# Performance work log

Measured on AMD Instinct MI355X. Metric: run time of the kernel, lower is better.

Reference implementation:

```python
import jax, jax.numpy as jnp
import numpy as np

EPS = 1e-5

def _bn(x, g, b, m, v):
    # x: [B, C, S]; per-channel affine batchnorm in eval mode
    scale = (g * jax.lax.rsqrt(v + EPS))[None, :, None]
    return (x - m[None, :, None]) * scale + b[None, :, None]

def setup_inputs() -> dict:
    key = jax.random.key(0)
    ks = jax.random.split(key, 32)
    B, C, H, W = 8, 512, 64, 32
    IC = 64        # inter_channel = 512 // 8
    S = H * W      # in_spatial = 2048
    IS = S // 8    # inter_spatial = 256
    DS = IS // 8   # down = 32
    randn = lambda k, shp: jax.random.normal(k, shp, dtype=jnp.float32)
    rand = lambda k, shp: jax.random.uniform(k, shp, dtype=jnp.float32)
    return {
        'x': randn(ks[0], (B, C, H, W)),
        'Wt': randn(ks[1], (IC, C)) * 0.05,
        'tg': rand(ks[2], (IC,)), 'tb': randn(ks[3], (IC,)) * 0.1,
        'tm': randn(ks[4], (IC,)) * 0.1, 'tv': rand(ks[5], (IC,)),
        'Wp': randn(ks[6], (IC, C)) * 0.05,
        'pg': rand(ks[7], (IC,)), 'pb': randn(ks[8], (IC,)) * 0.1,
        'pm': randn(ks[9], (IC,)) * 0.1, 'pv': rand(ks[10], (IC,)),
        'Wgg': randn(ks[11], (IS, 2 * S)) * 0.02,
        'ggg': rand(ks[12], (IS,)), 'ggb': randn(ks[13], (IS,)) * 0.1,
        'ggm': randn(ks[14], (IS,)) * 0.1, 'ggv': rand(ks[15], (IS,)),
        'W1': randn(ks[16], (DS, IS)) * 0.05,
        'w1g': rand(ks[17], (DS,)), 'w1b': randn(ks[18], (DS,)) * 0.1,
        'w1m': randn(ks[19], (DS,)) * 0.1, 'w1v': rand(ks[20], (DS,)),
        'W2': randn(ks[21], (1, DS)) * 0.1,
        'w2g': rand(ks[22], (1,)), 'w2b': randn(ks[23], (1,)) * 0.1,
        'w2m': randn(ks[24], (1,)) * 0.1, 'w2v': rand(ks[25], (1,)),
    }

def reference(x, Wt, tg, tb, tm, tv, Wp, pg, pb, pm, pv,
              Wgg, ggg, ggb, ggm, ggv, W1, w1g, w1b, w1m, w1v,
              W2, w2g, w2b, w2m, w2v):
    B, C, H, W = x.shape
    S = H * W
    xf = x.reshape(B, C, S)
    # theta / phi: 1x1 conv + BN + ReLU -> [B, IC, S]
    theta = jax.nn.relu(_bn(jnp.einsum('oc,bcs->bos', Wt, xf), tg, tb, tm, tv))
    phi = jax.nn.relu(_bn(jnp.einsum('oc,bcs->bos', Wp, xf), pg, pb, pm, pv))
    # spatial affinity: Gs[b,s,t] = sum_c theta[b,c,s] * phi[b,c,t]
    Gs = jnp.einsum('bcs,bct->bst', theta, phi)          # [B, S, S]
    # Gs_in = Gs^T (channels=phi-spatial), Gs_out = Gs (channels=theta-spatial)
    joint = jnp.concatenate([jnp.swapaxes(Gs, 1, 2), Gs], axis=1)  # [B, 2S, S]
    g = jax.nn.relu(_bn(jnp.einsum('oc,bcs->bos', Wgg, joint), ggg, ggb, ggm, ggv))
    y = jax.nn.relu(_bn(jnp.einsum('oc,bcs->bos', W1, g), w1g, w1b, w1m, w1v))
    ys = _bn(jnp.einsum('oc,bcs->bos', W2, y), w2g, w2b, w2m, w2v)  # [B, 1, S]
    gate = jax.nn.sigmoid(ys).reshape(B, 1, H, W)
    return x * gate
```

## Files before the change

kernel.cpp:

```cpp
#include <hip/hip_runtime.h>
#include <math.h>

#define EPS 1e-5f
#define B_ 8
#define C_ 512
#define S_ 2048
#define IC_ 64
#define IS_ 256
#define DS_ 32

#define OFF_THT   1024
#define OFF_PHT   (OFF_THT + S_*C_)
#define OFF_A     (OFF_PHT + S_*C_)
#define OFF_G     (OFF_A + 2*IS_*C_)
#define OFF_AP    OFF_G

using short8 = __attribute__((ext_vector_type(8))) short;
using f32x4  = __attribute__((ext_vector_type(4))) float;

__device__ __forceinline__ short f2bf(float f) {
  union { float f; unsigned u; } v; v.f = f;
  unsigned r = v.u + 0x7fffu + ((v.u >> 16) & 1u);
  return (short)(r >> 16);
}
__device__ __forceinline__ float bf2f(short h) {
  union { unsigned u; float f; } v;
  v.u = ((unsigned)(unsigned short)h) << 16;
  return v.f;
}
__device__ __forceinline__ void split8arr(const float* f, short8& hi, short8& lo) {
#pragma unroll
  for (int e = 0; e < 8; ++e) {
    short h = f2bf(f[e]);
    hi[e] = h;
    lo[e] = f2bf(f[e] - bf2f(h));
  }
}
__device__ __forceinline__ void split44(float4 a, float4 b, short8& hi, short8& lo) {
  float f[8] = {a.x, a.y, a.z, a.w, b.x, b.y, b.z, b.w};
  split8arr(f, hi, lo);
}

__global__ __launch_bounds__(512) void k1_mfma(
    const float* __restrict__ x, const float* __restrict__ Wt,
    const float* __restrict__ Wp,
    const float* __restrict__ tg, const float* __restrict__ tb,
    const float* __restrict__ tm, const float* __restrict__ tv,
    const float* __restrict__ pg, const float* __restrict__ pb,
    const float* __restrict__ pm, const float* __restrict__ pv,
    float* __restrict__ thetaT, float* __restrict__ phiT) {
  __shared__ short xh[64 * 72], xlo[64 * 72];
  __shared__ short wh[2][64 * 72], wlo[2][64 * 72];
  __shared__ float cst_l[256];
  const int tid  = threadIdx.x;
  const int lane = tid & 63;
  const int wv   = tid >> 6;
  const int mat  = wv >> 2, sh = wv & 3;
  const int s0   = blockIdx.x * 64;
  const int b    = blockIdx.y;
  const float* xb = x + (size_t)b * C_ * S_;
  const int xs = tid & 63;
  const int xo = tid >> 6;

  if (tid < 64) {
    float a = tg[tid] * rsqrtf(tv[tid] + EPS);
    cst_l[tid] = a; cst_l[64 + tid] = tb[tid] - tm[tid] * a;
    float ap = pg[tid] * rsqrtf(pv[tid] + EPS);
    cst_l[128 + tid] = ap; cst_l[192 + tid] = pb[tid] - pm[tid] * ap;
  }

  float  xr[8];
  float4 wr[2][2];
  f32x4  acc[4];
#pragma unroll
  for (int i = 0; i < 4; ++i) acc[i] = (f32x4){0.f, 0.f, 0.f, 0.f};

#define K1_PF(KC) do {                                                        \
    _Pragma("unroll")                                                         \
    for (int e = 0; e < 8; ++e)                                               \
      xr[e] = xb[(size_t)((KC) + xo * 8 + e) * S_ + s0 + xs];                 \
    _Pragma("unroll")                                                         \
    for (int p = 0; p < 2; ++p) {                                             \
      int q = tid + p * 512;                                                  \
      int mq = q >> 9, m = (q >> 3) & 63, oct = q & 7;                        \
      const float* Wm = mq ? Wp : Wt;                                         \
      wr[p][0] = *(const float4*)&Wm[(size_t)m * C_ + (KC) + oct * 8];        \
      wr[p][1] = *(const float4*)&Wm[(size_t)m * C_ + (KC) + oct * 8 + 4];    \
    } } while (0)

  K1_PF(0);
  for (int c = 0; c < 8; ++c) {
    if (c) __syncthreads();
    {
      short8 hi, lo; split8arr(xr, hi, lo);
      *(short8*)&xh[xs * 72 + xo * 8]  = hi;
      *(short8*)&xlo[xs * 72 + xo * 8] = lo;
    }
#pragma unroll
    for (int p = 0; p < 2; ++p) {
      int q = tid + p * 512;
      int mq = q >> 9, m = (q >> 3) & 63, oct = q & 7;
      short8 hi, lo; split44(wr[p][0], wr[p][1], hi, lo);
      *(short8*)&wh[mq][m * 72 + oct * 8]  = hi;
      *(short8*)&wlo[mq][m * 72 + oct * 8] = lo;
    }
    __syncthreads();
    if (c < 7) K1_PF((c + 1) * 64);
#pragma unroll
    for (int ks = 0; ks < 2; ++ks) {
      const int ko = ks * 32 + ((lane >> 4) << 3);
      short8 bh, bl, ah[4], al[4];
      {
        int r = (sh * 16 + (lane & 15)) * 72 + ko;
        bh = *(const short8*)&xh[r];
        bl = *(const short8*)&xlo[r];
      }
#pragma unroll
      for (int mi = 0; mi < 4; ++mi) {
        int r = (mi * 16 + (lane & 15)) * 72 + ko;
        ah[mi] = *(const short8*)&wh[mat][r];
        al[mi] = *(const short8*)&wlo[mat][r];
      }
#pragma unroll
      for (int mi = 0; mi < 4; ++mi) {
        acc[mi] = __builtin_amdgcn_mfma_f32_16x16x32_bf16(ah[mi], bh, acc[mi], 0, 0, 0);
        acc[mi] = __builtin_amdgcn_mfma_f32_16x16x32_bf16(ah[mi], bl, acc[mi], 0, 0, 0);
        acc[mi] = __builtin_amdgcn_mfma_f32_16x16x32_bf16(al[mi], bh, acc[mi], 0, 0, 0);
      }
    }
  }
#undef K1_PF
  const float* ac = &cst_l[mat * 128];
  float* outT = mat ? phiT : thetaT;
  const int s = s0 + sh * 16 + (lane & 15);
#pragma unroll
  for (int mi = 0; mi < 4; ++mi) {
    const int m = mi * 16 + ((lane >> 4) << 2);
    float4 sc4 = *(const float4*)&ac[m];
    float4 bi4 = *(const float4*)&ac[64 + m];
    float4 q;
    q.x = fmaxf(sc4.x * acc[mi][0] + bi4.x, 0.f);
    q.y = fmaxf(sc4.y * acc[mi][1] + bi4.y, 0.f);
    q.z = fmaxf(sc4.z * acc[mi][2] + bi4.z, 0.f);
    q.w = fmaxf(sc4.w * acc[mi][3] + bi4.w, 0.f);
    *(float4*)&outT[(size_t)s * C_ + b * IC_ + m] = q;
  }
}

__global__ __launch_bounds__(256) void k2_mfma(
    const float* __restrict__ Wgg, const float* __restrict__ ws,
    float* __restrict__ Ap) {
  __shared__ short nh[64 * 72], nlo[64 * 72];
  __shared__ short oh[128 * 72], olo[128 * 72];
  const int tid  = threadIdx.x;
  const int lane = tid & 63;
  const int wv   = tid >> 6;
  const int n0    = blockIdx.x * 64;
  const int o_blk = blockIdx.y * 128;
  const int mat   = blockIdx.z >> 3;
  const int part  = blockIdx.z & 7;
  const int t0 = part * 256;
  const float* Bm = ws + (mat ? OFF_THT : OFF_PHT);
  const int xs = tid & 63;
  const int xo = tid >> 6;

  float  ar[16];
  float4 br[4][2];
  f32x4  acc[4][2];
#pragma unroll
  for (int i = 0; i < 4; ++i)
#pragma unroll
    for (int j = 0; j < 2; ++j) acc[i][j] = (f32x4){0.f, 0.f, 0.f, 0.f};

#define K2_PF(KC) do {                                                        \
    _Pragma("unroll")                                                         \
    for (int h = 0; h < 2; ++h) {                                             \
      int oct = xo + h * 4;                                                   \
      _Pragma("unroll")                                                       \
      for (int e = 0; e < 8; ++e)                                             \
        ar[h * 8 + e] = Bm[(size_t)(t0 + (KC) + oct * 8 + e) * C_ + n0 + xs]; \
    }                                                                         \
    _Pragma("unroll")                                                         \
    for (int p = 0; p < 4; ++p) {                                             \
      int q = tid + p * 256;                                                  \
      int o = q >> 3, oct = q & 7;                                            \
      const float* src = &Wgg[(size_t)(o_blk + o) * (2 * S_) + mat * S_ +     \
                              t0 + (KC) + oct * 8];                           \
      br[p][0] = *(const float4*)src;                                         \
      br[p][1] = *(const float4*)(src + 4);                                   \
    } } while (0)

  K2_PF(0);
  for (int c = 0; c < 4; ++c) {
    if (c) __syncthreads();
#pragma unroll
    for (int h = 0; h < 2; ++h) {
      int oct = xo + h * 4;
      short8 hi, lo; split8arr(&ar[h * 8], hi, lo);
      *(short8*)&nh[xs * 72 + oct * 8]  = hi;
      *(short8*)&nlo[xs * 72 + oct * 8] = lo;
    }
#pragma unroll
    for (int p = 0; p < 4; ++p) {
      int q = tid + p * 256;
      int o = q >> 3, oct = q & 7;
      short8 hi, lo; split44(br[p][0], br[p][1], hi, lo);
      *(short8*)&oh[o * 72 + oct * 8]  = hi;
      *(short8*)&olo[o * 72 + oct * 8] = lo;
    }
    __syncthreads();
    if (c < 3) K2_PF((c + 1) * 64);
#pragma unroll
    for (int ks = 0; ks < 2; ++ks) {
      const int ko = ks * 32 + ((lane >> 4) << 3);
      short8 ah[4], al[4], bh[2], bl[2];
#pragma unroll
      for (int ni = 0; ni < 4; ++ni) {
        int r = (ni * 16 + (lane & 15)) * 72 + ko;
        ah[ni] = *(const short8*)&nh[r];
        al[ni] = *(const short8*)&nlo[r];
      }
#pragma unroll
      for (int oj = 0; oj < 2; ++oj) {
        int r = (wv * 32 + oj * 16 + (lane & 15)) * 72 + ko;
        bh[oj] = *(const short8*)&oh[r];
        bl[oj] = *(const short8*)&olo[r];
      }
#pragma unroll
      for (int ni = 0; ni < 4; ++ni)
#pragma unroll
        for (int oj = 0; oj < 2; ++oj) {
          acc[ni][oj] = __builtin_amdgcn_mfma_f32_16x16x32_bf16(
              ah[ni], bh[oj], acc[ni][oj], 0, 0, 0);
          acc[ni][oj] = __builtin_amdgcn_mfma_f32_16x16x32_bf16(
              ah[ni], bl[oj], acc[ni][oj], 0, 0, 0);
          acc[ni][oj] = __builtin_amdgcn_mfma_f32_16x16x32_bf16(
              al[ni], bh[oj], acc[ni][oj], 0, 0, 0);
        }
    }
  }
#undef K2_PF
#pragma unroll
  for (int ni = 0; ni < 4; ++ni) {
    const int nq = n0 + ni * 16 + ((lane >> 4) << 2);
#pragma unroll
    for (int oj = 0; oj < 2; ++oj) {
      int o = o_blk + wv * 32 + oj * 16 + (lane & 15);
      float4 q;
      q.x = acc[ni][oj][0]; q.y = acc[ni][oj][1];
      q.z = acc[ni][oj][2]; q.w = acc[ni][oj][3];
      *(float4*)&Ap[((size_t)(part * 2 + mat) * IS_ + o) * C_ + nq] = q;
    }
  }
}

__global__ __launch_bounds__(256) void k2b_reduce(float* __restrict__ ws) {
  int f = blockIdx.x * 256 + threadIdx.x;
  const float4* ap = (const float4*)(ws + OFF_AP);
  float4* a = (float4*)(ws + OFF_A);
  float4 s = ap[f];
#pragma unroll
  for (int p = 1; p < 8; ++p) {
    float4 t = ap[f + p * 65536];
    s.x += t.x; s.y += t.y; s.z += t.z; s.w += t.w;
  }
  a[f] = s;
}

__global__ __launch_bounds__(256) void k3_mfma(
    float* __restrict__ ws,
    const float* __restrict__ gg, const float* __restrict__ gb,
    const float* __restrict__ gm, const float* __restrict__ gv) {
  __shared__ short th[64 * 72], tlo[64 * 72];
  __shared__ short ohh[128 * 72], olo[128 * 72];
  __shared__ float cstg[512];
  const int tid  = threadIdx.x;
  const int lane = tid & 63;
  const int wv   = tid >> 6;
  const int s0    = blockIdx.x * 64;
  const int o_blk = blockIdx.y * 128;
  const int b     = blockIdx.z;
  const float* A = ws + OFF_A;

  {
    float a = gg[tid] * rsqrtf(gv[tid] + EPS);
    cstg[tid] = a; cstg[256 + tid] = gb[tid] - gm[tid] * a;
  }

  float4 ar[2][2];
  float4 br[4][2];
  f32x4  acc[4][2];
#pragma unroll
  for (int i = 0; i < 4; ++i)
#pragma unroll
    for (int j = 0; j < 2; ++j) acc[i][j] = (f32x4){0.f, 0.f, 0.f, 0.f};

#define K3_PF(MAT) do {                                                       \
    const float* Tsrc = ws + ((MAT) ? OFF_PHT : OFF_THT);                     \
    _Pragma("unroll")                                                         \
    for (int p = 0; p < 2; ++p) {                                             \
      int q = tid + p * 256;                                                  \
      int sl = q >> 3, oct = q & 7;                                           \
      const float* src = &Tsrc[(size_t)(s0 + sl) * C_ + b * IC_ + oct * 8];   \
      ar[p][0] = *(const float4*)src;                                         \
      ar[p][1] = *(const float4*)(src + 4);                                   \
    }                                                                         \
    _Pragma("unroll")                                                         \
    for (int p = 0; p < 4; ++p) {                                             \
      int q = tid + p * 256;                                                  \
      int o = q >> 3, oct = q & 7;                                            \
      const float* src = &A[((size_t)(MAT) * IS_ + o_blk + o) * C_ +          \
                            b * IC_ + oct * 8];                               \
      br[p][0] = *(const float4*)src;                                         \
      br[p][1] = *(const float4*)(src + 4);                                   \
    } } while (0)

  K3_PF(0);
  for (int c = 0; c < 2; ++c) {
    if (c) __syncthreads();
#pragma unroll
    for (int p = 0; p < 2; ++p) {
      int q = tid + p * 256;
      int sl = q >> 3, oct = q & 7;
      short8 hi, lo; split44(ar[p][0], ar[p][1], hi, lo);
      *(short8*)&th[sl * 72 + oct * 8]  = hi;
      *(short8*)&tlo[sl * 72 + oct * 8] = lo;
    }
#pragma unroll
    for (int p = 0; p < 4; ++p) {
      int q = tid + p * 256;
      int o = q >> 3, oct = q & 7;
      short8 hi, lo; split44(br[p][0], br[p][1], hi, lo);
      *(short8*)&ohh[o * 72 + oct * 8] = hi;
      *(short8*)&olo[o * 72 + oct * 8] = lo;
    }
    __syncthreads();
    if (c < 1) K3_PF(1);
#pragma unroll
    for (int ks = 0; ks < 2; ++ks) {
      const int ko = ks * 32 + ((lane >> 4) << 3);
      short8 ah[4], al[4], bh[2], bl[2];
#pragma unroll
      for (int si = 0; si < 4; ++si) {
        int r = (si * 16 + (lane & 15)) * 72 + ko;
        ah[si] = *(const short8*)&th[r];
        al[si] = *(const short8*)&tlo[r];
      }
#pragma unroll
      for (int oj = 0; oj < 2; ++oj) {
        int r = (wv * 32 + oj * 16 + (lane & 15)) * 72 + ko;
        bh[oj] = *(const short8*)&ohh[r];
        bl[oj] = *(const short8*)&olo[r];
      }
#pragma unroll
      for (int si = 0; si < 4; ++si)
#pragma unroll
        for (int oj = 0; oj < 2; ++oj) {
          acc[si][oj] = __builtin_amdgcn_mfma_f32_16x16x32_bf16(
              ah[si], bh[oj], acc[si][oj], 0, 0, 0);
          acc[si][oj] = __builtin_amdgcn_mfma_f32_16x16x32_bf16(
              ah[si], bl[oj], acc[si][oj], 0, 0, 0);
          acc[si][oj] = __builtin_amdgcn_mfma_f32_16x16x32_bf16(
              al[si], bh[oj], acc[si][oj], 0, 0, 0);
        }
    }
  }
#undef K3_PF
  float* g = ws + OFF_G;
#pragma unroll
  for (int oj = 0; oj < 2; ++oj) {
    int o = o_blk + wv * 32 + oj * 16 + (lane & 15);
    float sc = cstg[o], bi = cstg[256 + o];
#pragma unroll
    for (int si = 0; si < 4; ++si) {
      int sq = s0 + si * 16 + ((lane >> 4) << 2);
      float4 q;
      q.x = fmaxf(sc * acc[si][oj][0] + bi, 0.f);
      q.y = fmaxf(sc * acc[si][oj][1] + bi, 0.f);
      q.z = fmaxf(sc * acc[si][oj][2] + bi, 0.f);
      q.w = fmaxf(sc * acc[si][oj][3] + bi, 0.f);
      *(float4*)&g[((size_t)b * IS_ + o) * S_ + sq] = q;
    }
  }
}

__global__ __launch_bounds__(512) void k4_fused(
    const float* __restrict__ x, const float* __restrict__ W1,
    const float* __restrict__ W2,
    const float* __restrict__ w1g, const float* __restrict__ w1b,
    const float* __restrict__ w1m, const float* __restrict__ w1v,
    const float* __restrict__ w2g, const float* __restrict__ w2b,
    const float* __restrict__ w2m, const float* __restrict__ w2v,
    const float* __restrict__ ws, float* __restrict__ out) {
  __shared__ float lds_g[128 * 65];
  __shared__ float lds_w[32 * 260];
  __shared__ float lds_y[32 * 65];
  __shared__ float lds_gate[64];
  __shared__ float wc[66];
  const int tid = threadIdx.x;
  const int s0  = blockIdx.x * 64;
  const int b   = blockIdx.y;
  const int s   = tid & 63;
  const int og  = tid >> 6;
  const float* gsrc = ws + OFF_G + (size_t)b * IS_ * S_;

  if (tid < 32) {
    float a = w1g[tid] * rsqrtf(w1v[tid] + EPS);
    wc[tid] = a; wc[32 + tid] = w1b[tid] - w1m[tid] * a;
  } else if (tid == 32) {
    float a = w2g[0] * rsqrtf(w2v[0] + EPS);
    wc[64] = a; wc[65] = w2b[0] - w2m[0] * a;
  }
#pragma unroll
  for (int j = 0; j < 4; ++j) {
    int f = tid + j * 512;
    int row = f >> 6, c4 = f & 63;
    *(float4*)&lds_w[row * 260 + c4 * 4] =
        *(const float4*)&W1[(size_t)row * IS_ + c4 * 4];
  }
  float acc[4] = {};

  for (int half = 0; half < 2; ++half) {
    __syncthreads();
#pragma unroll
    for (int j = 0; j < 16; ++j) {
      int idx = tid + j * 512;
      lds_g[(idx >> 6) * 65 + (idx & 63)] =
          gsrc[(size_t)(half * 128 + (idx >> 6)) * S_ + s0 + (idx & 63)];
    }
    __syncthreads();
#pragma unroll
    for (int c4 = 0; c4 < 32; ++c4) {
      float g0 = lds_g[(c4 * 4 + 0) * 65 + s];
      float g1 = lds_g[(c4 * 4 + 1) * 65 + s];
      float g2 = lds_g[(c4 * 4 + 2) * 65 + s];
      float g3 = lds_g[(c4 * 4 + 3) * 65 + s];
#pragma unroll
      for (int j = 0; j < 4; ++j) {
        const float4 w = *(const float4*)&lds_w[(og * 4 + j) * 260 +
                                                half * 128 + c4 * 4];
        acc[j] += g0 * w.x + g1 * w.y + g2 * w.z + g3 * w.w;
      }
    }
  }
#pragma unroll
  for (int j = 0; j < 4; ++j) {
    int o = og * 4 + j;
    float v = wc[o] * acc[j] + wc[32 + o];
    lds_y[o * 65 + s] = v > 0.f ? v : 0.f;
  }
  __syncthreads();
  if (tid < 64) {
    float sum = 0.f;
#pragma unroll
    for (int c = 0; c < 32; ++c) sum += W2[c] * lds_y[c * 65 + tid];
    float ys = wc[64] * sum + wc[65];
    lds_gate[tid] = 1.f / (1.f + expf(-ys));
  }
  __syncthreads();
  const int l = tid & 63, w = tid >> 6;
  const int q4 = (l & 15) * 4;
  const int cl = w * 4 + (l >> 4);
  const float4 gv = *(const float4*)&lds_gate[q4];
  const float* xb = x + (size_t)b * C_ * S_ + s0;
  float* ob = out + (size_t)b * C_ * S_ + s0;
#pragma unroll
  for (int it = 0; it < 16; ++it) {
    int ch = it * 32 + cl;
    const float4 xv = *(const float4*)&xb[(size_t)ch * S_ + q4];
    float4 ov;
    ov.x = xv.x * gv.x; ov.y = xv.y * gv.y;
    ov.z = xv.z * gv.z; ov.w = xv.w * gv.w;
    *(float4*)&ob[(size_t)ch * S_ + q4] = ov;
  }
}

extern "C" void kernel_launch(void* const* d_in, const int* in_sizes, int n_in,
                              void* d_out, int out_size, void* d_ws, size_t ws_size,
                              hipStream_t stream) {
  const float* x   = (const float*)d_in[0];
  const float* Wt  = (const float*)d_in[1];
  const float* tg  = (const float*)d_in[2];
  const float* tb  = (const float*)d_in[3];
  const float* tm  = (const float*)d_in[4];
  const float* tv  = (const float*)d_in[5];
  const float* Wp  = (const float*)d_in[6];
  const float* pg  = (const float*)d_in[7];
  const float* pb  = (const float*)d_in[8];
  const float* pm  = (const float*)d_in[9];
  const float* pv  = (const float*)d_in[10];
  const float* Wgg = (const float*)d_in[11];
  const float* ggg = (const float*)d_in[12];
  const float* ggb = (const float*)d_in[13];
  const float* ggm = (const float*)d_in[14];
  const float* ggv = (const float*)d_in[15];
  const float* W1  = (const float*)d_in[16];
  const float* w1g = (const float*)d_in[17];
  const float* w1b = (const float*)d_in[18];
  const float* w1m = (const float*)d_in[19];
  const float* w1v = (const float*)d_in[20];
  const float* W2  = (const float*)d_in[21];
  const float* w2g = (const float*)d_in[22];
  const float* w2b = (const float*)d_in[23];
  const float* w2m = (const float*)d_in[24];
  const float* w2v = (const float*)d_in[25];
  float* ws  = (float*)d_ws;
  float* out = (float*)d_out;

  k1_mfma<<<dim3(32, 8), 512, 0, stream>>>(
      x, Wt, Wp, tg, tb, tm, tv, pg, pb, pm, pv,
      ws + OFF_THT, ws + OFF_PHT);
  k2_mfma<<<dim3(8, 2, 16), 256, 0, stream>>>(Wgg, ws, ws + OFF_AP);
  k2b_reduce<<<256, 256, 0, stream>>>(ws);
  k3_mfma<<<dim3(32, 2, 8), 256, 0, stream>>>(ws, ggg, ggb, ggm, ggv);
  k4_fused<<<dim3(32, 8), 512, 0, stream>>>(
      x, W1, W2, w1g, w1b, w1m, w1v, w2g, w2b, w2m, w2v, ws, out);
}
```

Baseline: 77.55 us.

## Store intermediates as pre-split bf16 hi/lo pairs instead of fp32

The theta/phi and reduced A intermediates are now written by their producer kernels as bf16 hi/lo pairs, so k2 and k3 no longer re-split fp32 tiles on every load. The g activation is written as a single bf16 and widened to fp32 in k4. This keeps the same traffic for the split tensors, removes repeated split arithmetic, and halves g traffic. The risk is the lower precision of g, which drops its lo part, along with scalar 2-byte gathers in k2's theta/phi loads.

```diff
diff --git a/kernel.cpp b/kernel.cpp
--- a/kernel.cpp
+++ b/kernel.cpp
@@ -9,13 +9,19 @@
 #define IS_ 256
 #define DS_ 32
 
-#define OFF_THT   1024
-#define OFF_PHT   (OFF_THT + S_*C_)
-#define OFF_A     (OFF_PHT + S_*C_)
-#define OFF_G     (OFF_A + 2*IS_*C_)
+#define SZ_T      (S_*C_/2)
+#define OFF_THT_H 1024
+#define OFF_THT_L (OFF_THT_H + SZ_T)
+#define OFF_PHT_H (OFF_THT_L + SZ_T)
+#define OFF_PHT_L (OFF_PHT_H + SZ_T)
+#define SZ_A      (2*IS_*C_/2)
+#define OFF_A_H   (OFF_PHT_L + SZ_T)
+#define OFF_A_L   (OFF_A_H + SZ_A)
+#define OFF_G     (OFF_A_L + SZ_A)
 #define OFF_AP    OFF_G
 
 using short8 = __attribute__((ext_vector_type(8))) short;
+using sh4    = __attribute__((ext_vector_type(4))) short;
 using f32x4  = __attribute__((ext_vector_type(4))) float;
 
 __device__ __forceinline__ short f2bf(float f) {
@@ -48,7 +54,7 @@
     const float* __restrict__ tm, const float* __restrict__ tv,
     const float* __restrict__ pg, const float* __restrict__ pb,
     const float* __restrict__ pm, const float* __restrict__ pv,
-    float* __restrict__ thetaT, float* __restrict__ phiT) {
+    float* __restrict__ ws) {
   __shared__ short xh[64 * 72], xlo[64 * 72];
   __shared__ short wh[2][64 * 72], wlo[2][64 * 72];
   __shared__ float cst_l[256];
@@ -131,19 +137,28 @@
   }
 #undef K1_PF
   const float* ac = &cst_l[mat * 128];
-  float* outT = mat ? phiT : thetaT;
+  short* outH = (short*)(ws + (mat ? OFF_PHT_H : OFF_THT_H));
+  short* outL = (short*)(ws + (mat ? OFF_PHT_L : OFF_THT_L));
   const int s = s0 + sh * 16 + (lane & 15);
 #pragma unroll
   for (int mi = 0; mi < 4; ++mi) {
     const int m = mi * 16 + ((lane >> 4) << 2);
     float4 sc4 = *(const float4*)&ac[m];
     float4 bi4 = *(const float4*)&ac[64 + m];
-    float4 q;
-    q.x = fmaxf(sc4.x * acc[mi][0] + bi4.x, 0.f);
-    q.y = fmaxf(sc4.y * acc[mi][1] + bi4.y, 0.f);
-    q.z = fmaxf(sc4.z * acc[mi][2] + bi4.z, 0.f);
-    q.w = fmaxf(sc4.w * acc[mi][3] + bi4.w, 0.f);
-    *(float4*)&outT[(size_t)s * C_ + b * IC_ + m] = q;
+    float vals[4];
+    vals[0] = fmaxf(sc4.x * acc[mi][0] + bi4.x, 0.f);
+    vals[1] = fmaxf(sc4.y * acc[mi][1] + bi4.y, 0.f);
+    vals[2] = fmaxf(sc4.z * acc[mi][2] + bi4.z, 0.f);
+    vals[3] = fmaxf(sc4.w * acc[mi][3] + bi4.w, 0.f);
+    sh4 qh, ql;
+#pragma unroll
+    for (int e = 0; e < 4; ++e) {
+      short h = f2bf(vals[e]);
+      qh[e] = h; ql[e] = f2bf(vals[e] - bf2f(h));
+    }
+    size_t ix = (size_t)s * C_ + b * IC_ + m;
+    *(sh4*)&outH[ix] = qh;
+    *(sh4*)&outL[ix] = ql;
   }
 }
 
@@ -160,11 +175,12 @@
   const int mat   = blockIdx.z >> 3;
   const int part  = blockIdx.z & 7;
   const int t0 = part * 256;
-  const float* Bm = ws + (mat ? OFF_THT : OFF_PHT);
+  const short* BmH = (const short*)(ws + (mat ? OFF_THT_H : OFF_PHT_H));
+  const short* BmL = (const short*)(ws + (mat ? OFF_THT_L : OFF_PHT_L));
   const int xs = tid & 63;
   const int xo = tid >> 6;
 
-  float  ar[16];
+  short8 arh[2], arl[2];
   float4 br[4][2];
   f32x4  acc[4][2];
 #pragma unroll
@@ -177,8 +193,11 @@
     for (int h = 0; h < 2; ++h) {                                             \
       int oct = xo + h * 4;                                                   \
       _Pragma("unroll")                                                       \
-      for (int e = 0; e < 8; ++e)                                             \
-        ar[h * 8 + e] = Bm[(size_t)(t0 + (KC) + oct * 8 + e) * C_ + n0 + xs]; \
+      for (int e = 0; e < 8; ++e) {                                           \
+        size_t ix = (size_t)(t0 + (KC) + oct * 8 + e) * C_ + n0 + xs;         \
+        arh[h][e] = BmH[ix];                                                  \
+        arl[h][e] = BmL[ix];                                                  \
+      }                                                                       \
     }                                                                         \
     _Pragma("unroll")                                                         \
     for (int p = 0; p < 4; ++p) {                                             \
@@ -196,9 +215,8 @@
 #pragma unroll
     for (int h = 0; h < 2; ++h) {
       int oct = xo + h * 4;
-      short8 hi, lo; split8arr(&ar[h * 8], hi, lo);
-      *(short8*)&nh[xs * 72 + oct * 8]  = hi;
-      *(short8*)&nlo[xs * 72 + oct * 8] = lo;
+      *(short8*)&nh[xs * 72 + oct * 8]  = arh[h];
+      *(short8*)&nlo[xs * 72 + oct * 8] = arl[h];
     }
 #pragma unroll
     for (int p = 0; p < 4; ++p) {
@@ -257,14 +275,21 @@
 __global__ __launch_bounds__(256) void k2b_reduce(float* __restrict__ ws) {
   int f = blockIdx.x * 256 + threadIdx.x;
   const float4* ap = (const float4*)(ws + OFF_AP);
-  float4* a = (float4*)(ws + OFF_A);
   float4 s = ap[f];
 #pragma unroll
   for (int p = 1; p < 8; ++p) {
     float4 t = ap[f + p * 65536];
     s.x += t.x; s.y += t.y; s.z += t.z; s.w += t.w;
   }
-  a[f] = s;
+  float vals[4] = {s.x, s.y, s.z, s.w};
+  sh4 h4, l4;
+#pragma unroll
+  for (int e = 0; e < 4; ++e) {
+    short h = f2bf(vals[e]);
+    h4[e] = h; l4[e] = f2bf(vals[e] - bf2f(h));
+  }
+  ((sh4*)(ws + OFF_A_H))[f] = h4;
+  ((sh4*)(ws + OFF_A_L))[f] = l4;
 }
 
 __global__ __launch_bounds__(256) void k3_mfma(
@@ -280,15 +305,16 @@
   const int s0    = blockIdx.x * 64;
   const int o_blk = blockIdx.y * 128;
   const int b     = blockIdx.z;
-  const float* A = ws + OFF_A;
+  const short* AH = (const short*)(ws + OFF_A_H);
+  const short* AL = (const short*)(ws + OFF_A_L);
 
   {
     float a = gg[tid] * rsqrtf(gv[tid] + EPS);
     cstg[tid] = a; cstg[256 + tid] = gb[tid] - gm[tid] * a;
   }
 
-  float4 ar[2][2];
-  float4 br[4][2];
+  short8 arh[2], arl[2];
+  short8 brh[4], brl[4];
   f32x4  acc[4][2];
 #pragma unroll
   for (int i = 0; i < 4; ++i)
@@ -296,23 +322,23 @@
     for (int j = 0; j < 2; ++j) acc[i][j] = (f32x4){0.f, 0.f, 0.f, 0.f};
 
 #define K3_PF(MAT) do {                                                       \
-    const float* Tsrc = ws + ((MAT) ? OFF_PHT : OFF_THT);                     \
+    const short* TH = (const short*)(ws + ((MAT) ? OFF_PHT_H : OFF_THT_H));   \
+    const short* TL = (const short*)(ws + ((MAT) ? OFF_PHT_L : OFF_THT_L));   \
     _Pragma("unroll")                                                         \
     for (int p = 0; p < 2; ++p) {                                             \
       int q = tid + p * 256;                                                  \
       int sl = q >> 3, oct = q & 7;                                           \
-      const float* src = &Tsrc[(size_t)(s0 + sl) * C_ + b * IC_ + oct * 8];   \
-      ar[p][0] = *(const float4*)src;                                         \
-      ar[p][1] = *(const float4*)(src + 4);                                   \
+      size_t ix = (size_t)(s0 + sl) * C_ + b * IC_ + oct * 8;                 \
+      arh[p] = *(const short8*)&TH[ix];                                       \
+      arl[p] = *(const short8*)&TL[ix];                                       \
     }                                                                         \
     _Pragma("unroll")                                                         \
     for (int p = 0; p < 4; ++p) {                                             \
       int q = tid + p * 256;                                                  \
       int o = q >> 3, oct = q & 7;                                            \
-      const float* src = &A[((size_t)(MAT) * IS_ + o_blk + o) * C_ +          \
-                            b * IC_ + oct * 8];                               \
-      br[p][0] = *(const float4*)src;                                         \
-      br[p][1] = *(const float4*)(src + 4);                                   \
+      size_t ix = ((size_t)(MAT) * IS_ + o_blk + o) * C_ + b * IC_ + oct * 8; \
+      brh[p] = *(const short8*)&AH[ix];                                       \
+      brl[p] = *(const short8*)&AL[ix];                                       \
     } } while (0)
 
   K3_PF(0);
@@ -322,17 +348,15 @@
     for (int p = 0; p < 2; ++p) {
       int q = tid + p * 256;
       int sl = q >> 3, oct = q & 7;
-      short8 hi, lo; split44(ar[p][0], ar[p][1], hi, lo);
-      *(short8*)&th[sl * 72 + oct * 8]  = hi;
-      *(short8*)&tlo[sl * 72 + oct * 8] = lo;
+      *(short8*)&th[sl * 72 + oct * 8]  = arh[p];
+      *(short8*)&tlo[sl * 72 + oct * 8] = arl[p];
     }
 #pragma unroll
     for (int p = 0; p < 4; ++p) {
       int q = tid + p * 256;
       int o = q >> 3, oct = q & 7;
-      short8 hi, lo; split44(br[p][0], br[p][1], hi, lo);
-      *(short8*)&ohh[o * 72 + oct * 8] = hi;
-      *(short8*)&olo[o * 72 + oct * 8] = lo;
+      *(short8*)&ohh[o * 72 + oct * 8] = brh[p];
+      *(short8*)&olo[o * 72 + oct * 8] = brl[p];
     }
     __syncthreads();
     if (c < 1) K3_PF(1);
@@ -366,7 +390,7 @@
     }
   }
 #undef K3_PF
-  float* g = ws + OFF_G;
+  short* g = (short*)(ws + OFF_G);
 #pragma unroll
   for (int oj = 0; oj < 2; ++oj) {
     int o = o_blk + wv * 32 + oj * 16 + (lane & 15);
@@ -374,12 +398,12 @@
 #pragma unroll
     for (int si = 0; si < 4; ++si) {
       int sq = s0 + si * 16 + ((lane >> 4) << 2);
-      float4 q;
-      q.x = fmaxf(sc * acc[si][oj][0] + bi, 0.f);
-      q.y = fmaxf(sc * acc[si][oj][1] + bi, 0.f);
-      q.z = fmaxf(sc * acc[si][oj][2] + bi, 0.f);
-      q.w = fmaxf(sc * acc[si][oj][3] + bi, 0.f);
-      *(float4*)&g[((size_t)b * IS_ + o) * S_ + sq] = q;
+      sh4 q4;
+      q4[0] = f2bf(fmaxf(sc * acc[si][oj][0] + bi, 0.f));
+      q4[1] = f2bf(fmaxf(sc * acc[si][oj][1] + bi, 0.f));
+      q4[2] = f2bf(fmaxf(sc * acc[si][oj][2] + bi, 0.f));
+      q4[3] = f2bf(fmaxf(sc * acc[si][oj][3] + bi, 0.f));
+      *(sh4*)&g[((size_t)b * IS_ + o) * S_ + sq] = q4;
     }
   }
 }
@@ -392,7 +416,7 @@
     const float* __restrict__ w2g, const float* __restrict__ w2b,
     const float* __restrict__ w2m, const float* __restrict__ w2v,
     const float* __restrict__ ws, float* __restrict__ out) {
-  __shared__ float lds_g[128 * 65];
+  __shared__ float lds_g[128 * 68];
   __shared__ float lds_w[32 * 260];
   __shared__ float lds_y[32 * 65];
   __shared__ float lds_gate[64];
@@ -402,7 +426,7 @@
   const int b   = blockIdx.y;
   const int s   = tid & 63;
   const int og  = tid >> 6;
-  const float* gsrc = ws + OFF_G + (size_t)b * IS_ * S_;
+  const short* gsrc = (const short*)(ws + OFF_G) + (size_t)b * IS_ * S_;
 
   if (tid < 32) {
     float a = w1g[tid] * rsqrtf(w1v[tid] + EPS);
@@ -423,18 +447,23 @@
   for (int half = 0; half < 2; ++half) {
     __syncthreads();
 #pragma unroll
-    for (int j = 0; j < 16; ++j) {
-      int idx = tid + j * 512;
-      lds_g[(idx >> 6) * 65 + (idx & 63)] =
-          gsrc[(size_t)(half * 128 + (idx >> 6)) * S_ + s0 + (idx & 63)];
+    for (int j = 0; j < 2; ++j) {
+      int ridx = tid + j * 512;
+      int row = ridx >> 3, oct = ridx & 7;
+      short8 v = *(const short8*)&gsrc[(size_t)(half * 128 + row) * S_ +
+                                       s0 + oct * 8];
+      float4 f0 = make_float4(bf2f(v[0]), bf2f(v[1]), bf2f(v[2]), bf2f(v[3]));
+      float4 f1 = make_float4(bf2f(v[4]), bf2f(v[5]), bf2f(v[6]), bf2f(v[7]));
+      *(float4*)&lds_g[row * 68 + oct * 8]     = f0;
+      *(float4*)&lds_g[row * 68 + oct * 8 + 4] = f1;
     }
     __syncthreads();
 #pragma unroll
     for (int c4 = 0; c4 < 32; ++c4) {
-      float g0 = lds_g[(c4 * 4 + 0) * 65 + s];
-      float g1 = lds_g[(c4 * 4 + 1) * 65 + s];
-      float g2 = lds_g[(c4 * 4 + 2) * 65 + s];
-      float g3 = lds_g[(c4 * 4 + 3) * 65 + s];
+      float g0 = lds_g[(c4 * 4 + 0) * 68 + s];
+      float g1 = lds_g[(c4 * 4 + 1) * 68 + s];
+      float g2 = lds_g[(c4 * 4 + 2) * 68 + s];
+      float g3 = lds_g[(c4 * 4 + 3) * 68 + s];
 #pragma unroll
       for (int j = 0; j < 4; ++j) {
         const float4 w = *(const float4*)&lds_w[(og * 4 + j) * 260 +
@@ -508,8 +537,7 @@
   float* out = (float*)d_out;
 
   k1_mfma<<<dim3(32, 8), 512, 0, stream>>>(
-      x, Wt, Wp, tg, tb, tm, tv, pg, pb, pm, pv,
-      ws + OFF_THT, ws + OFF_PHT);
+      x, Wt, Wp, tg, tb, tm, tv, pg, pb, pm, pv, ws);
   k2_mfma<<<dim3(8, 2, 16), 256, 0, stream>>>(Wgg, ws, ws + OFF_AP);
   k2b_reduce<<<256, 256, 0, stream>>>(ws);
   k3_mfma<<<dim3(32, 2, 8), 256, 0, stream>>>(ws, ggg, ggb, ggm, ggv);
```

Result: faster. 69.73 us (-10.1%).
